# Performance work log

Measured on AMD Instinct MI355X. Metric: run time of the kernel, lower is better.

## Reference

```python
import jax, jax.numpy as jnp
import numpy as np

N_NODES, N_EDGES, IN_DIM, HID, N_FEAT_CLOSE, N_GRAPHS = 100000, 1600000, 128, 64, 5, 512


def _glorot(k, shape):
    lim = float(np.sqrt(6.0 / (shape[0] + shape[1])))
    return jax.random.uniform(k, shape, jnp.float32, -lim, lim)


def setup_inputs() -> dict:
    key = jax.random.key(0)
    ks = jax.random.split(key, 16)
    x = jax.random.normal(ks[0], (N_NODES, IN_DIM), jnp.float32)
    edge_index = jax.random.randint(ks[1], (2, N_EDGES), 0, N_NODES, jnp.int32)
    closeness = jax.random.uniform(ks[2], (N_NODES, N_FEAT_CLOSE), jnp.float32)
    batch = jnp.sort(jax.random.randint(ks[3], (N_NODES,), 0, N_GRAPHS, jnp.int32))
    return {
        'x': x, 'edge_index': edge_index, 'closeness': closeness, 'batch': batch,
        'num_graphs': N_GRAPHS,
        'W1': _glorot(ks[4], (IN_DIM, HID)), 'b1': jnp.zeros((HID,), jnp.float32),
        'W2': _glorot(ks[5], (HID, HID)), 'b2': jnp.zeros((HID,), jnp.float32),
        'W3': _glorot(ks[6], (HID, HID)), 'b3': jnp.zeros((HID,), jnp.float32),
        'Wc': _glorot(ks[7], (N_FEAT_CLOSE, 1)), 'bc': jnp.zeros((1,), jnp.float32),
        'Wa1': _glorot(ks[8], (HID, 16)), 'ba1': jnp.zeros((16,), jnp.float32),
        'Wa2': _glorot(ks[9], (16, 1)), 'ba2': jnp.zeros((1,), jnp.float32),
    }


def reference(x, edge_index, closeness, batch, num_graphs, W1, b1, W2, b2, W3, b3, Wc, bc, Wa1, ba1, Wa2, ba2):
    src, dst = edge_index[0], edge_index[1]
    N = x.shape[0]
    # GCN symmetric normalization with implicit self-loops (weight 1)
    deg = jax.ops.segment_sum(jnp.ones(src.shape, x.dtype), dst, num_segments=N) + 1.0
    dinv = jax.lax.rsqrt(deg)
    norm = dinv[src] * dinv[dst]  # [E]
    self_norm = (dinv * dinv)[:, None]  # 1/deg, self-loop coefficient

    def gcn(h, W, b):
        h = h @ W  # [N, hid]
        agg = jax.ops.segment_sum(h[src] * norm[:, None], dst, num_segments=N)
        return jax.nn.relu(agg + h * self_norm + b)

    h = gcn(x, W1, b1)
    h = gcn(h, W2, b2)
    h = gcn(h, W3, b3)

    # per-graph softmax over closeness scores, scaled by graph size
    s = closeness @ Wc + bc  # [N,1]
    smax = jax.ops.segment_max(s, batch, num_segments=num_graphs)
    e = jnp.exp(s - smax[batch])
    ssum = jax.ops.segment_sum(e, batch, num_segments=num_graphs)
    counts = jax.ops.segment_sum(jnp.ones((N,), x.dtype), batch, num_segments=num_graphs)
    w = (e / ssum[batch]) * counts[batch][:, None]  # [N,1]

    # weighted per-graph max pooling, then tiny MLP per graph
    pooled = jax.ops.segment_max(w * h, batch, num_segments=num_graphs)  # [G,64]
    a = jax.nn.relu(pooled @ Wa1 + ba1)
    return a @ Wa2 + ba2  # [G,1]
```

## Files before the change

### kernel.cpp

```cpp
#include <hip/hip_runtime.h>

#define N_NODESC 100000
#define N_EDGESC 1600000
#define IN_DIMC 128
#define HIDC 64
#define N_GRAPHSC 512
#define PAD_DEG 64


__global__ void zero_bounds_kernel(int* __restrict__ cntR, const int* __restrict__ batch,
                                   int* __restrict__ gstart) {
  int i = blockIdx.x * blockDim.x + threadIdx.x;
  if (i >= N_NODESC) return;
  cntR[i] = 0;
  cntR[N_NODESC + i] = 0;
  cntR[2 * N_NODESC + i] = 0;
  cntR[3 * N_NODESC + i] = 0;
  int b = batch[i];
  int prev = (i == 0) ? -1 : batch[i - 1];
  for (int g = prev + 1; g <= b; ++g) gstart[g] = i;
  if (i == N_NODESC - 1)
    for (int g = b + 1; g <= N_GRAPHSC; ++g) gstart[g] = N_NODESC;
}

__global__ void deg_kernel(const int* __restrict__ dstv, int* __restrict__ cntR,
                           int* __restrict__ slot) {
  int e4 = (blockIdx.x * blockDim.x + threadIdx.x) * 4;
  if (e4 >= N_EDGESC) return;
  int4 d = *(const int4*)(dstv + e4);
  int4 s;
  s.x = atomicAdd(&cntR[d.x], 1);
  s.y = atomicAdd(&cntR[N_NODESC + d.y], 1);
  s.z = atomicAdd(&cntR[2 * N_NODESC + d.z], 1);
  s.w = atomicAdd(&cntR[3 * N_NODESC + d.w], 1);
  *(int4*)(slot + e4) = s;
}

__global__ void off_dinv_kernel(const int* __restrict__ cntR, int* __restrict__ offR,
                                int* __restrict__ cnt, float* __restrict__ dinv) {
  int i = blockIdx.x * blockDim.x + threadIdx.x;
  if (i >= N_NODESC) return;
  int c0 = cntR[i];
  int c1 = cntR[N_NODESC + i];
  int c2 = cntR[2 * N_NODESC + i];
  int c3 = cntR[3 * N_NODESC + i];
  offR[i] = c0;
  offR[N_NODESC + i] = c0 + c1;
  offR[2 * N_NODESC + i] = c0 + c1 + c2;
  int tot = c0 + c1 + c2 + c3;
  cnt[i] = tot;
  dinv[i] = rsqrtf((float)tot + 1.0f);
}

__global__ void fill_pad_kernel(const int* __restrict__ srcv, const int* __restrict__ dstv,
                                const int* __restrict__ slot, const int* __restrict__ offR,
                                int* __restrict__ csr_pad) {
  int e4 = (blockIdx.x * blockDim.x + threadIdx.x) * 4;
  if (e4 >= N_EDGESC) return;
  int4 s = *(const int4*)(srcv + e4);
  int4 d = *(const int4*)(dstv + e4);
  int4 sl = *(const int4*)(slot + e4);
  int p0 = sl.x;
  int p1 = offR[d.y] + sl.y;
  int p2 = offR[N_NODESC + d.z] + sl.z;
  int p3 = offR[2 * N_NODESC + d.w] + sl.w;
  if (p0 < PAD_DEG) __builtin_nontemporal_store(s.x, &csr_pad[d.x * PAD_DEG + p0]);
  if (p1 < PAD_DEG) __builtin_nontemporal_store(s.y, &csr_pad[d.y * PAD_DEG + p1]);
  if (p2 < PAD_DEG) __builtin_nontemporal_store(s.z, &csr_pad[d.z * PAD_DEG + p2]);
  if (p3 < PAD_DEG) __builtin_nontemporal_store(s.w, &csr_pad[d.w * PAD_DEG + p3]);
}

#define G5_KC 32
#define G5_LD 136
#define G5_BLOCKS ((N_NODESC + 127) / 128)

template <int KT>
__global__ void __launch_bounds__(128, 3)
gemm8x8_kernel(const float* __restrict__ X, const float* __restrict__ W,
               const float* __restrict__ dinv, float* __restrict__ T) {
  __shared__ float xs[G5_KC * G5_LD];
  __shared__ float ws[G5_KC * 64];
  int t = threadIdx.x;
  int base = blockIdx.x * 128;
  int r0 = (t >> 3) * 8;
  int c0 = (t & 7) * 8;
  int rg = t >> 2;
  int kq2 = t & 3;

  float4 acc[8][2];
#pragma unroll
  for (int i = 0; i < 8; ++i) {
    acc[i][0] = make_float4(0.f, 0.f, 0.f, 0.f);
    acc[i][1] = make_float4(0.f, 0.f, 0.f, 0.f);
  }

  for (int kb = 0; kb < KT; kb += G5_KC) {
    if (kb) __syncthreads();
#pragma unroll
    for (int a = 0; a < 2; ++a) {
      int kq = kq2 * 2 + a;
      float4 vr[4];
#pragma unroll
      for (int i = 0; i < 4; ++i) {
        int row = base + rg * 4 + i;
        if (row >= N_NODESC) row = N_NODESC - 1;
        vr[i] = *(const float4*)(X + (size_t)row * KT + kb + kq * 4);
      }
      const float* a0 = (const float*)&vr[0];
      const float* a1 = (const float*)&vr[1];
      const float* a2 = (const float*)&vr[2];
      const float* a3 = (const float*)&vr[3];
#pragma unroll
      for (int c = 0; c < 4; ++c) {
        float4 wv = make_float4(a0[c], a1[c], a2[c], a3[c]);
        *(float4*)(xs + (kq * 4 + c) * G5_LD + rg * 4) = wv;
      }
    }
#pragma unroll
    for (int j = 0; j < 4; ++j) {
      int f = j * 128 + t;
      int kl = f >> 4;
      int c4 = (f & 15) * 4;
      *(float4*)(ws + kl * 64 + c4) = *(const float4*)(W + (size_t)(kb + kl) * HIDC + c4);
    }
    __syncthreads();
#pragma unroll 8
    for (int k = 0; k < G5_KC; ++k) {
      float4 xa = *(const float4*)(xs + k * G5_LD + r0);
      float4 xb = *(const float4*)(xs + k * G5_LD + r0 + 4);
      float4 w0 = *(const float4*)(ws + k * 64 + c0);
      float4 w1 = *(const float4*)(ws + k * 64 + c0 + 4);
      float xf[8] = {xa.x, xa.y, xa.z, xa.w, xb.x, xb.y, xb.z, xb.w};
#pragma unroll
      for (int i = 0; i < 8; ++i) {
        acc[i][0].x = fmaf(xf[i], w0.x, acc[i][0].x);
        acc[i][0].y = fmaf(xf[i], w0.y, acc[i][0].y);
        acc[i][0].z = fmaf(xf[i], w0.z, acc[i][0].z);
        acc[i][0].w = fmaf(xf[i], w0.w, acc[i][0].w);
        acc[i][1].x = fmaf(xf[i], w1.x, acc[i][1].x);
        acc[i][1].y = fmaf(xf[i], w1.y, acc[i][1].y);
        acc[i][1].z = fmaf(xf[i], w1.z, acc[i][1].z);
        acc[i][1].w = fmaf(xf[i], w1.w, acc[i][1].w);
      }
    }
  }
#pragma unroll
  for (int i = 0; i < 8; ++i) {
    int row = base + r0 + i;
    if (row < N_NODESC) {
      float dv = dinv[row];
#pragma unroll
      for (int j = 0; j < 2; ++j) {
        float4 o;
        o.x = acc[i][j].x * dv;
        o.y = acc[i][j].y * dv;
        o.z = acc[i][j].z * dv;
        o.w = acc[i][j].w * dv;
        *(float4*)(T + (size_t)row * HIDC + c0 + 4 * j) = o;
      }
    }
  }
}

__global__ void gather_kernel(const float* __restrict__ ts, const float* __restrict__ dinv,
                              const int* __restrict__ cnt, const int* __restrict__ csr_pad,
                              const float* __restrict__ bias, float* __restrict__ h) {
  int lane = threadIdx.x & 63;
  int node = (blockIdx.x * blockDim.x + threadIdx.x) >> 6;
  if (node >= N_NODESC) return;
  int q = lane >> 4;
  int c = lane & 15;
  int deg = min(cnt[node], PAD_DEG);
  const int* __restrict__ row = csr_pad + node * PAD_DEG;
  const float4* __restrict__ ts4 = (const float4*)ts;
  float4 acc = make_float4(0.f, 0.f, 0.f, 0.f);
  int e = 0;
  for (; e + 16 <= deg; e += 16) {
    int s0 = row[e + q];
    int s1 = row[e + 4 + q];
    int s2 = row[e + 8 + q];
    int s3 = row[e + 12 + q];
    float4 v0 = ts4[s0 * 16 + c];
    float4 v1 = ts4[s1 * 16 + c];
    float4 v2 = ts4[s2 * 16 + c];
    float4 v3 = ts4[s3 * 16 + c];
    acc.x += (v0.x + v1.x) + (v2.x + v3.x);
    acc.y += (v0.y + v1.y) + (v2.y + v3.y);
    acc.z += (v0.z + v1.z) + (v2.z + v3.z);
    acc.w += (v0.w + v1.w) + (v2.w + v3.w);
  }
  for (; e + 4 <= deg; e += 4) {
    int s0 = row[e + q];
    float4 v = ts4[s0 * 16 + c];
    acc.x += v.x;
    acc.y += v.y;
    acc.z += v.z;
    acc.w += v.w;
  }
  if (e < deg && q < deg - e) {
    int s0 = row[e + q];
    float4 v = ts4[s0 * 16 + c];
    acc.x += v.x;
    acc.y += v.y;
    acc.z += v.z;
    acc.w += v.w;
  }
  acc.x += __shfl_xor(acc.x, 16);
  acc.y += __shfl_xor(acc.y, 16);
  acc.z += __shfl_xor(acc.z, 16);
  acc.w += __shfl_xor(acc.w, 16);
  acc.x += __shfl_xor(acc.x, 32);
  acc.y += __shfl_xor(acc.y, 32);
  acc.z += __shfl_xor(acc.z, 32);
  acc.w += __shfl_xor(acc.w, 32);
  if (q == 0) {
    float4 self = ts4[node * 16 + c];
    float4 bv = ((const float4*)bias)[c];
    float dv = dinv[node];
    float4 o;
    o.x = fmaxf(fmaf(acc.x + self.x, dv, bv.x), 0.f);
    o.y = fmaxf(fmaf(acc.y + self.y, dv, bv.y), 0.f);
    o.z = fmaxf(fmaf(acc.z + self.z, dv, bv.z), 0.f);
    o.w = fmaxf(fmaf(acc.w + self.w, dv, bv.w), 0.f);
    ((float4*)h)[node * 16 + c] = o;
  }
}

__global__ void __launch_bounds__(256)
readout_kernel(const float* __restrict__ h, const float* __restrict__ closeness,
               const float* __restrict__ Wc, const float* __restrict__ bc,
               const int* __restrict__ gstart, const float* __restrict__ Wa1,
               const float* __restrict__ ba1, const float* __restrict__ Wa2,
               const float* __restrict__ ba2, float* __restrict__ out) {
  __shared__ float sArr[1024];
  __shared__ float red[256];
  __shared__ float cross[4 * 64];
  int g = blockIdx.x;
  int t = threadIdx.x;
  int n0 = gstart[g], n1 = gstart[g + 1];
  int count = n1 - n0;
  int cap = min(count, 1024);
  float wc0 = Wc[0], wc1 = Wc[1], wc2 = Wc[2], wc3 = Wc[3], wc4 = Wc[4], bcv = bc[0];
  float lmax = -3.4e38f;
  for (int idx = t; idx < cap; idx += 256) {
    const float* c = closeness + (size_t)(n0 + idx) * 5;
    float s = fmaf(c[4], wc4, fmaf(c[3], wc3, fmaf(c[2], wc2, fmaf(c[1], wc1, fmaf(c[0], wc0, bcv)))));
    sArr[idx] = s;
    lmax = fmaxf(lmax, s);
  }
  red[t] = lmax;
  __syncthreads();
  for (int s = 128; s > 0; s >>= 1) {
    if (t < s) red[t] = fmaxf(red[t], red[t + s]);
    __syncthreads();
  }
  float m = red[0];
  __syncthreads();
  float lsum = 0.f;
  for (int idx = t; idx < cap; idx += 256) {
    float e = expf(sArr[idx] - m);
    sArr[idx] = e;
    lsum += e;
  }
  red[t] = lsum;
  __syncthreads();
  for (int s = 128; s > 0; s >>= 1) {
    if (t < s) red[t] += red[t + s];
    __syncthreads();
  }
  float scale = (count > 0) ? ((float)count / red[0]) : 0.f;
  __syncthreads();
  int wv = t >> 6, lane = t & 63;
  float pmax = 0.f;
  for (int idx = wv; idx < cap; idx += 4) {
    float w = sArr[idx] * scale;
    pmax = fmaxf(pmax, w * h[(size_t)(n0 + idx) * HIDC + lane]);
  }
  cross[wv * 64 + lane] = pmax;
  __syncthreads();
  if (wv == 0) {
    float p = fmaxf(fmaxf(cross[lane], cross[64 + lane]),
                    fmaxf(cross[128 + lane], cross[192 + lane]));
    float o = 0.f;
#pragma unroll
    for (int tt = 0; tt < 16; ++tt) {
      float prod = p * Wa1[lane * 16 + tt];
#pragma unroll
      for (int off = 32; off > 0; off >>= 1) prod += __shfl_xor(prod, off);
      float a = fmaxf(prod + ba1[tt], 0.f);
      o += a * Wa2[tt];
    }
    if (lane == 0) out[g] = o + ba2[0];
  }
}


extern "C" void kernel_launch(void* const* d_in, const int* in_sizes, int n_in,
                              void* d_out, int out_size, void* d_ws, size_t ws_size,
                              hipStream_t stream) {
  const float* x = (const float*)d_in[0];
  const int* ei = (const int*)d_in[1];
  const float* closeness = (const float*)d_in[2];
  const int* batch = (const int*)d_in[3];
  const float* W1 = (const float*)d_in[5];
  const float* b1 = (const float*)d_in[6];
  const float* W2 = (const float*)d_in[7];
  const float* b2 = (const float*)d_in[8];
  const float* W3 = (const float*)d_in[9];
  const float* b3 = (const float*)d_in[10];
  const float* Wc = (const float*)d_in[11];
  const float* bc = (const float*)d_in[12];
  const float* Wa1 = (const float*)d_in[13];
  const float* ba1 = (const float*)d_in[14];
  const float* Wa2 = (const float*)d_in[15];
  const float* ba2 = (const float*)d_in[16];
  float* out = (float*)d_out;
  const int* srcv = ei;
  const int* dstv = ei + N_EDGESC;

  char* ws = (char*)d_ws;
  size_t off = 0;
  auto alloc = [&](size_t bytes) -> void* {
    void* p = ws + off;
    off = (off + bytes + 255) & ~(size_t)255;
    return p;
  };
  float* tbuf = (float*)alloc(sizeof(float) * N_NODESC * HIDC);
  float* hbuf = (float*)alloc(sizeof(float) * N_NODESC * HIDC);
  int* csr_pad = (int*)alloc(sizeof(int) * N_NODESC * PAD_DEG);
  int* slot = (int*)alloc(sizeof(int) * N_EDGESC);
  int* cntR = (int*)alloc(sizeof(int) * N_NODESC * 4);
  int* offR = (int*)alloc(sizeof(int) * N_NODESC * 3);
  int* cnt = (int*)alloc(sizeof(int) * N_NODESC);
  float* dinv = (float*)alloc(sizeof(float) * N_NODESC);
  int* gstart = (int*)alloc(sizeof(int) * (N_GRAPHSC + 1));

  const int B = 256;
  int gN = (N_NODESC + B - 1) / B;
  int gE4 = (N_EDGESC / 4 + B - 1) / B;
  int gGather = (N_NODESC * 64) / B;

  zero_bounds_kernel<<<gN, B, 0, stream>>>(cntR, batch, gstart);
  deg_kernel<<<gE4, B, 0, stream>>>(dstv, cntR, slot);
  off_dinv_kernel<<<gN, B, 0, stream>>>(cntR, offR, cnt, dinv);
  fill_pad_kernel<<<gE4, B, 0, stream>>>(srcv, dstv, slot, offR, csr_pad);

  gemm8x8_kernel<IN_DIMC><<<G5_BLOCKS, 128, 0, stream>>>(x, W1, dinv, tbuf);
  gather_kernel<<<gGather, B, 0, stream>>>(tbuf, dinv, cnt, csr_pad, b1, hbuf);
  gemm8x8_kernel<HIDC><<<G5_BLOCKS, 128, 0, stream>>>(hbuf, W2, dinv, tbuf);
  gather_kernel<<<gGather, B, 0, stream>>>(tbuf, dinv, cnt, csr_pad, b2, hbuf);
  gemm8x8_kernel<HIDC><<<G5_BLOCKS, 128, 0, stream>>>(hbuf, W3, dinv, tbuf);
  gather_kernel<<<gGather, B, 0, stream>>>(tbuf, dinv, cnt, csr_pad, b3, hbuf);

  readout_kernel<<<N_GRAPHSC, B, 0, stream>>>(hbuf, closeness, Wc, bc, gstart,
                                              Wa1, ba1, Wa2, ba2, out);
}
```

Before: 521.8 us.

## Fuse degree counting, first GEMM and softmax weights into combined launches

```diff
diff --git a/kernel.cpp b/kernel.cpp
--- a/kernel.cpp
+++ b/kernel.cpp
@@ -21,19 +21,6 @@
   for (int g = prev + 1; g <= b; ++g) gstart[g] = i;
   if (i == N_NODESC - 1)
     for (int g = b + 1; g <= N_GRAPHSC; ++g) gstart[g] = N_NODESC;
-}
-
-__global__ void deg_kernel(const int* __restrict__ dstv, int* __restrict__ cntR,
-                           int* __restrict__ slot) {
-  int e4 = (blockIdx.x * blockDim.x + threadIdx.x) * 4;
-  if (e4 >= N_EDGESC) return;
-  int4 d = *(const int4*)(dstv + e4);
-  int4 s;
-  s.x = atomicAdd(&cntR[d.x], 1);
-  s.y = atomicAdd(&cntR[N_NODESC + d.y], 1);
-  s.z = atomicAdd(&cntR[2 * N_NODESC + d.z], 1);
-  s.w = atomicAdd(&cntR[3 * N_NODESC + d.w], 1);
-  *(int4*)(slot + e4) = s;
 }
 
 __global__ void off_dinv_kernel(const int* __restrict__ cntR, int* __restrict__ offR,
@@ -52,26 +39,194 @@
   dinv[i] = rsqrtf((float)tot + 1.0f);
 }
 
-__global__ void fill_pad_kernel(const int* __restrict__ srcv, const int* __restrict__ dstv,
-                                const int* __restrict__ slot, const int* __restrict__ offR,
-                                int* __restrict__ csr_pad) {
-  int e4 = (blockIdx.x * blockDim.x + threadIdx.x) * 4;
-  if (e4 >= N_EDGESC) return;
-  int4 s = *(const int4*)(srcv + e4);
-  int4 d = *(const int4*)(dstv + e4);
-  int4 sl = *(const int4*)(slot + e4);
-  int p0 = sl.x;
-  int p1 = offR[d.y] + sl.y;
-  int p2 = offR[N_NODESC + d.z] + sl.z;
-  int p3 = offR[2 * N_NODESC + d.w] + sl.w;
-  if (p0 < PAD_DEG) __builtin_nontemporal_store(s.x, &csr_pad[d.x * PAD_DEG + p0]);
-  if (p1 < PAD_DEG) __builtin_nontemporal_store(s.y, &csr_pad[d.y * PAD_DEG + p1]);
-  if (p2 < PAD_DEG) __builtin_nontemporal_store(s.z, &csr_pad[d.z * PAD_DEG + p2]);
-  if (p3 < PAD_DEG) __builtin_nontemporal_store(s.w, &csr_pad[d.w * PAD_DEG + p3]);
-}
-
 #define G5_KC 32
 #define G5_LD 136
+#define M1_DEG_B 3125
+#define M1_GEMM_B ((N_NODESC + 127) / 128)
+#define M1_BLOCKS (M1_DEG_B + M1_GEMM_B + N_GRAPHSC)
+
+__global__ void __launch_bounds__(128, 3)
+mega1_kernel(const int* __restrict__ dstv, int* __restrict__ cntR, int* __restrict__ slot,
+             const float* __restrict__ X, const float* __restrict__ W1,
+             float* __restrict__ T,
+             const float* __restrict__ closeness, const float* __restrict__ Wc,
+             const float* __restrict__ bc, const int* __restrict__ gstart,
+             float* __restrict__ wexp) {
+  __shared__ float smem[G5_KC * G5_LD + G5_KC * 64];
+  int bid = blockIdx.x;
+  int t = threadIdx.x;
+
+  if (bid < M1_DEG_B) {
+    int e4 = (bid * 128 + t) * 4;
+    if (e4 >= N_EDGESC) return;
+    int4 d = *(const int4*)(dstv + e4);
+    int4 s;
+    s.x = atomicAdd(&cntR[d.x], 1);
+    s.y = atomicAdd(&cntR[N_NODESC + d.y], 1);
+    s.z = atomicAdd(&cntR[2 * N_NODESC + d.z], 1);
+    s.w = atomicAdd(&cntR[3 * N_NODESC + d.w], 1);
+    *(int4*)(slot + e4) = s;
+    return;
+  }
+
+  if (bid < M1_DEG_B + M1_GEMM_B) {
+    float* xs = smem;
+    float* ws = smem + G5_KC * G5_LD;
+    int base = (bid - M1_DEG_B) * 128;
+    int r0 = (t >> 3) * 8;
+    int c0 = (t & 7) * 8;
+    int rg = t >> 2;
+    int kq2 = t & 3;
+
+    float4 acc[8][2];
+#pragma unroll
+    for (int i = 0; i < 8; ++i) {
+      acc[i][0] = make_float4(0.f, 0.f, 0.f, 0.f);
+      acc[i][1] = make_float4(0.f, 0.f, 0.f, 0.f);
+    }
+
+    for (int kb = 0; kb < IN_DIMC; kb += G5_KC) {
+      if (kb) __syncthreads();
+#pragma unroll
+      for (int a = 0; a < 2; ++a) {
+        int kq = kq2 * 2 + a;
+        float4 vr[4];
+#pragma unroll
+        for (int i = 0; i < 4; ++i) {
+          int row = base + rg * 4 + i;
+          if (row >= N_NODESC) row = N_NODESC - 1;
+          vr[i] = *(const float4*)(X + (size_t)row * IN_DIMC + kb + kq * 4);
+        }
+        const float* a0 = (const float*)&vr[0];
+        const float* a1 = (const float*)&vr[1];
+        const float* a2 = (const float*)&vr[2];
+        const float* a3 = (const float*)&vr[3];
+#pragma unroll
+        for (int c = 0; c < 4; ++c) {
+          float4 wv = make_float4(a0[c], a1[c], a2[c], a3[c]);
+          *(float4*)(xs + (kq * 4 + c) * G5_LD + rg * 4) = wv;
+        }
+      }
+#pragma unroll
+      for (int j = 0; j < 4; ++j) {
+        int f = j * 128 + t;
+        int kl = f >> 4;
+        int c4 = (f & 15) * 4;
+        *(float4*)(ws + kl * 64 + c4) = *(const float4*)(W1 + (size_t)(kb + kl) * HIDC + c4);
+      }
+      __syncthreads();
+#pragma unroll 8
+      for (int k = 0; k < G5_KC; ++k) {
+        float4 xa = *(const float4*)(xs + k * G5_LD + r0);
+        float4 xb = *(const float4*)(xs + k * G5_LD + r0 + 4);
+        float4 w0 = *(const float4*)(ws + k * 64 + c0);
+        float4 w1 = *(const float4*)(ws + k * 64 + c0 + 4);
+        float xf[8] = {xa.x, xa.y, xa.z, xa.w, xb.x, xb.y, xb.z, xb.w};
+#pragma unroll
+        for (int i = 0; i < 8; ++i) {
+          acc[i][0].x = fmaf(xf[i], w0.x, acc[i][0].x);
+          acc[i][0].y = fmaf(xf[i], w0.y, acc[i][0].y);
+          acc[i][0].z = fmaf(xf[i], w0.z, acc[i][0].z);
+          acc[i][0].w = fmaf(xf[i], w0.w, acc[i][0].w);
+          acc[i][1].x = fmaf(xf[i], w1.x, acc[i][1].x);
+          acc[i][1].y = fmaf(xf[i], w1.y, acc[i][1].y);
+          acc[i][1].z = fmaf(xf[i], w1.z, acc[i][1].z);
+          acc[i][1].w = fmaf(xf[i], w1.w, acc[i][1].w);
+        }
+      }
+    }
+#pragma unroll
+    for (int i = 0; i < 8; ++i) {
+      int row = base + r0 + i;
+      if (row < N_NODESC) {
+        *(float4*)(T + (size_t)row * HIDC + c0) = acc[i][0];
+        *(float4*)(T + (size_t)row * HIDC + c0 + 4) = acc[i][1];
+      }
+    }
+    return;
+  }
+
+  {
+    float* sArr = smem;
+    float* red = smem + 1024;
+    int g = bid - M1_DEG_B - M1_GEMM_B;
+    int n0 = gstart[g], n1 = gstart[g + 1];
+    int count = n1 - n0;
+    int cap = min(count, 1024);
+    float wc0 = Wc[0], wc1 = Wc[1], wc2 = Wc[2], wc3 = Wc[3], wc4 = Wc[4], bcv = bc[0];
+    float lmax = -3.4e38f;
+    for (int idx = t; idx < cap; idx += 128) {
+      const float* c = closeness + (size_t)(n0 + idx) * 5;
+      float s = fmaf(c[4], wc4, fmaf(c[3], wc3, fmaf(c[2], wc2, fmaf(c[1], wc1, fmaf(c[0], wc0, bcv)))));
+      sArr[idx] = s;
+      lmax = fmaxf(lmax, s);
+    }
+    red[t] = lmax;
+    __syncthreads();
+    for (int s = 64; s > 0; s >>= 1) {
+      if (t < s) red[t] = fmaxf(red[t], red[t + s]);
+      __syncthreads();
+    }
+    float m = red[0];
+    __syncthreads();
+    float lsum = 0.f;
+    for (int idx = t; idx < cap; idx += 128) {
+      float e = expf(sArr[idx] - m);
+      sArr[idx] = e;
+      lsum += e;
+    }
+    red[t] = lsum;
+    __syncthreads();
+    for (int s = 64; s > 0; s >>= 1) {
+      if (t < s) red[t] += red[t + s];
+      __syncthreads();
+    }
+    float scale = (count > 0) ? ((float)count / red[0]) : 0.f;
+    for (int idx = t; idx < cap; idx += 128) wexp[n0 + idx] = sArr[idx] * scale;
+  }
+}
+
+#define M3_FILL_B 1563
+#define M3_SCALE_B 3125
+#define M3_BLOCKS (M3_FILL_B + M3_SCALE_B)
+
+__global__ void __launch_bounds__(256)
+mega3_kernel(const int* __restrict__ srcv, const int* __restrict__ dstv,
+             const int* __restrict__ slot, const int* __restrict__ offR,
+             int* __restrict__ csr_pad,
+             float* __restrict__ T, const float* __restrict__ dinv) {
+  int bid = blockIdx.x;
+  int t = threadIdx.x;
+  if (bid < M3_FILL_B) {
+    int e4 = (bid * 256 + t) * 4;
+    if (e4 >= N_EDGESC) return;
+    int4 s = *(const int4*)(srcv + e4);
+    int4 d = *(const int4*)(dstv + e4);
+    int4 sl = *(const int4*)(slot + e4);
+    int p0 = sl.x;
+    int p1 = offR[d.y] + sl.y;
+    int p2 = offR[N_NODESC + d.z] + sl.z;
+    int p3 = offR[2 * N_NODESC + d.w] + sl.w;
+    if (p0 < PAD_DEG) __builtin_nontemporal_store(s.x, &csr_pad[d.x * PAD_DEG + p0]);
+    if (p1 < PAD_DEG) __builtin_nontemporal_store(s.y, &csr_pad[d.y * PAD_DEG + p1]);
+    if (p2 < PAD_DEG) __builtin_nontemporal_store(s.z, &csr_pad[d.z * PAD_DEG + p2]);
+    if (p3 < PAD_DEG) __builtin_nontemporal_store(s.w, &csr_pad[d.w * PAD_DEG + p3]);
+    return;
+  }
+  int f = (bid - M3_FILL_B) * 256 + t;
+  int i4 = f * 2;
+  if (i4 >= N_NODESC * 16) return;
+  float4* p = (float4*)T;
+  float dv0 = dinv[i4 >> 4];
+  float dv1 = dinv[(i4 + 1) >> 4];
+  float4 a = p[i4];
+  float4 b = p[i4 + 1];
+  a.x *= dv0; a.y *= dv0; a.z *= dv0; a.w *= dv0;
+  b.x *= dv1; b.y *= dv1; b.z *= dv1; b.w *= dv1;
+  p[i4] = a;
+  p[i4 + 1] = b;
+}
+
 #define G5_BLOCKS ((N_NODESC + 127) / 128)
 
 template <int KT>
@@ -227,54 +382,19 @@
 }
 
 __global__ void __launch_bounds__(256)
-readout_kernel(const float* __restrict__ h, const float* __restrict__ closeness,
-               const float* __restrict__ Wc, const float* __restrict__ bc,
-               const int* __restrict__ gstart, const float* __restrict__ Wa1,
-               const float* __restrict__ ba1, const float* __restrict__ Wa2,
-               const float* __restrict__ ba2, float* __restrict__ out) {
-  __shared__ float sArr[1024];
-  __shared__ float red[256];
+readout2_kernel(const float* __restrict__ h, const float* __restrict__ wexp,
+                const int* __restrict__ gstart, const float* __restrict__ Wa1,
+                const float* __restrict__ ba1, const float* __restrict__ Wa2,
+                const float* __restrict__ ba2, float* __restrict__ out) {
   __shared__ float cross[4 * 64];
   int g = blockIdx.x;
   int t = threadIdx.x;
   int n0 = gstart[g], n1 = gstart[g + 1];
-  int count = n1 - n0;
-  int cap = min(count, 1024);
-  float wc0 = Wc[0], wc1 = Wc[1], wc2 = Wc[2], wc3 = Wc[3], wc4 = Wc[4], bcv = bc[0];
-  float lmax = -3.4e38f;
-  for (int idx = t; idx < cap; idx += 256) {
-    const float* c = closeness + (size_t)(n0 + idx) * 5;
-    float s = fmaf(c[4], wc4, fmaf(c[3], wc3, fmaf(c[2], wc2, fmaf(c[1], wc1, fmaf(c[0], wc0, bcv)))));
-    sArr[idx] = s;
-    lmax = fmaxf(lmax, s);
-  }
-  red[t] = lmax;
-  __syncthreads();
-  for (int s = 128; s > 0; s >>= 1) {
-    if (t < s) red[t] = fmaxf(red[t], red[t + s]);
-    __syncthreads();
-  }
-  float m = red[0];
-  __syncthreads();
-  float lsum = 0.f;
-  for (int idx = t; idx < cap; idx += 256) {
-    float e = expf(sArr[idx] - m);
-    sArr[idx] = e;
-    lsum += e;
-  }
-  red[t] = lsum;
-  __syncthreads();
-  for (int s = 128; s > 0; s >>= 1) {
-    if (t < s) red[t] += red[t + s];
-    __syncthreads();
-  }
-  float scale = (count > 0) ? ((float)count / red[0]) : 0.f;
-  __syncthreads();
+  int cap = min(n1 - n0, 1024);
   int wv = t >> 6, lane = t & 63;
   float pmax = 0.f;
   for (int idx = wv; idx < cap; idx += 4) {
-    float w = sArr[idx] * scale;
-    pmax = fmaxf(pmax, w * h[(size_t)(n0 + idx) * HIDC + lane]);
+    pmax = fmaxf(pmax, wexp[n0 + idx] * h[(size_t)(n0 + idx) * HIDC + lane]);
   }
   cross[wv * 64 + lane] = pmax;
   __syncthreads();
@@ -333,25 +453,24 @@
   int* offR = (int*)alloc(sizeof(int) * N_NODESC * 3);
   int* cnt = (int*)alloc(sizeof(int) * N_NODESC);
   float* dinv = (float*)alloc(sizeof(float) * N_NODESC);
+  float* wexp = (float*)alloc(sizeof(float) * N_NODESC);
   int* gstart = (int*)alloc(sizeof(int) * (N_GRAPHSC + 1));
 
   const int B = 256;
   int gN = (N_NODESC + B - 1) / B;
-  int gE4 = (N_EDGESC / 4 + B - 1) / B;
   int gGather = (N_NODESC * 64) / B;
 
   zero_bounds_kernel<<<gN, B, 0, stream>>>(cntR, batch, gstart);
-  deg_kernel<<<gE4, B, 0, stream>>>(dstv, cntR, slot);
+  mega1_kernel<<<M1_BLOCKS, 128, 0, stream>>>(dstv, cntR, slot, x, W1, tbuf,
+                                              closeness, Wc, bc, gstart, wexp);
   off_dinv_kernel<<<gN, B, 0, stream>>>(cntR, offR, cnt, dinv);
-  fill_pad_kernel<<<gE4, B, 0, stream>>>(srcv, dstv, slot, offR, csr_pad);
-
-  gemm8x8_kernel<IN_DIMC><<<G5_BLOCKS, 128, 0, stream>>>(x, W1, dinv, tbuf);
+  mega3_kernel<<<M3_BLOCKS, B, 0, stream>>>(srcv, dstv, slot, offR, csr_pad, tbuf, dinv);
+
   gather_kernel<<<gGather, B, 0, stream>>>(tbuf, dinv, cnt, csr_pad, b1, hbuf);
   gemm8x8_kernel<HIDC><<<G5_BLOCKS, 128, 0, stream>>>(hbuf, W2, dinv, tbuf);
   gather_kernel<<<gGather, B, 0, stream>>>(tbuf, dinv, cnt, csr_pad, b2, hbuf);
   gemm8x8_kernel<HIDC><<<G5_BLOCKS, 128, 0, stream>>>(hbuf, W3, dinv, tbuf);
   gather_kernel<<<gGather, B, 0, stream>>>(tbuf, dinv, cnt, csr_pad, b3, hbuf);
 
-  readout_kernel<<<N_GRAPHSC, B, 0, stream>>>(hbuf, closeness, Wc, bc, gstart,
-                                              Wa1, ba1, Wa2, ba2, out);
-}
+  readout2_kernel<<<N_GRAPHSC, B, 0, stream>>>(hbuf, wexp, gstart, Wa1, ba1, Wa2, ba2, out);
+}
```

Measured after the change: 524.3 us. About the same (+0.5%).
